# Kernel optimization log

Measured on AMD Instinct MI355X. Metric: run time of the kernel, lower is better.

Reference implementation:

```python
import jax, jax.numpy as jnp
import numpy as np
from jax import lax

Z_DIM = 64
ZS_SIZE = [[1, 1]] * 12 + [[2, 1]] + [[2, 2]] * 11 + [[4, 2]] + [[4, 4]] * 11  # 36 embeddings
FILTER = [[16, 16]] * 6 + [[16, 32]] + [[32, 32]] * 5 + [[32, 64]] + [[64, 64]] * 5  # 18 blocks
OFFS = np.cumsum([0] + [h * k for h, k in ZS_SIZE]).tolist()  # 242 z-vectors total


def _hyper(Z, hn_w2, hn_b2, hn_w1, hn_b1):
    # Batched HyperNetwork: Z [n, 64] -> kernels [n, 16, 16, 3, 3]
    n = Z.shape[0]
    h_in = (Z @ hn_w2 + hn_b2).reshape(n, 16, Z_DIM)            # [n, 16, 64]
    h_fin = jnp.einsum('nid,do->nio', h_in, hn_w1) + hn_b1       # [n, 16, 144]
    return h_fin.reshape(n, 16, 16, 3, 3)


def _make_w(z_all, idx, hn_w2, hn_b2, hn_w1, hn_b1):
    # Assemble conv weight [h*16, k*16, 3, 3] from h*k hypernet tiles (cat dim=1 over k, dim=0 over h)
    h, k = ZS_SIZE[idx]
    Z = z_all[OFFS[idx]:OFFS[idx] + h * k]
    K = _hyper(Z, hn_w2, hn_b2, hn_w1, hn_b1)                    # [h*k, 16, 16, 3, 3]
    K = K.reshape(h, k, 16, 16, 3, 3).transpose(0, 2, 1, 3, 4, 5)
    return K.reshape(h * 16, k * 16, 3, 3)


def _conv(x, w, stride, pad):
    return lax.conv_general_dilated(x, w, (stride, stride), [(pad, pad), (pad, pad)],
                                    dimension_numbers=('NCHW', 'OIHW', 'NCHW'))


def _bn(x, i, g, b, m, v):
    # eval-mode BatchNorm2d with running stats; params padded to 64 channels
    C = x.shape[1]
    gg = g[i, :C].reshape(1, C, 1, 1)
    bb = b[i, :C].reshape(1, C, 1, 1)
    mm = m[i, :C].reshape(1, C, 1, 1)
    vv = v[i, :C].reshape(1, C, 1, 1)
    return (x - mm) * (gg * lax.rsqrt(vv + 1e-5)) + bb


def setup_inputs() -> dict:
    key = jax.random.key(0)
    ks = jax.random.split(key, 16)
    B = 1024
    x = jax.random.normal(ks[0], (B, 3, 32, 32), jnp.float32)
    conv1_w = jax.random.normal(ks[1], (16, 3, 3, 3), jnp.float32) / np.float32(np.sqrt(27.0))
    conv1_b = jnp.zeros((16,), jnp.float32)
    n_bn = 37  # bn1 + 2 per block
    bn_gamma = jnp.ones((n_bn, 64), jnp.float32)
    bn_beta = jnp.zeros((n_bn, 64), jnp.float32)
    bn_mean = jnp.zeros((n_bn, 64), jnp.float32)
    bn_var = jnp.ones((n_bn, 64), jnp.float32)
    hn_w2 = jax.random.normal(ks[2], (Z_DIM, 16 * Z_DIM), jnp.float32) * 0.04
    hn_b2 = jax.random.normal(ks[3], (16 * Z_DIM,), jnp.float32) * 0.01
    hn_w1 = jax.random.normal(ks[4], (Z_DIM, 16 * 9), jnp.float32) * 0.04
    hn_b1 = jax.random.normal(ks[5], (16 * 9,), jnp.float32) * 0.01
    z_all = jax.random.normal(ks[6], (OFFS[-1], Z_DIM), jnp.float32)
    res_w6 = jax.random.normal(ks[7], (32, 16, 1, 1), jnp.float32) * 0.25
    res_b6 = jnp.zeros((32,), jnp.float32)
    res_w12 = jax.random.normal(ks[8], (64, 32, 1, 1), jnp.float32) * 0.18
    res_b12 = jnp.zeros((64,), jnp.float32)
    fin_w = jax.random.normal(ks[9], (10, 64), jnp.float32) * 0.1
    fin_b = jnp.zeros((10,), jnp.float32)
    return {"x": x, "conv1_w": conv1_w, "conv1_b": conv1_b,
            "bn_gamma": bn_gamma, "bn_beta": bn_beta, "bn_mean": bn_mean, "bn_var": bn_var,
            "hn_w2": hn_w2, "hn_b2": hn_b2, "hn_w1": hn_w1, "hn_b1": hn_b1,
            "z_all": z_all, "res_w6": res_w6, "res_b6": res_b6,
            "res_w12": res_w12, "res_b12": res_b12, "fin_w": fin_w, "fin_b": fin_b}


def reference(x, conv1_w, conv1_b, bn_gamma, bn_beta, bn_mean, bn_var,
              hn_w2, hn_b2, hn_w1, hn_b1, z_all,
              res_w6, res_b6, res_w12, res_b12, fin_w, fin_b):
    x = _conv(x, conv1_w, 1, 1) + conv1_b.reshape(1, -1, 1, 1)
    x = jax.nn.relu(_bn(x, 0, bn_gamma, bn_beta, bn_mean, bn_var))
    for i in range(18):
        w1 = _make_w(z_all, 2 * i, hn_w2, hn_b2, hn_w1, hn_b1)
        w2 = _make_w(z_all, 2 * i + 1, hn_w2, hn_b2, hn_w1, hn_b1)
        down = (i > 5 and i % 6 == 0)
        if down:
            rw, rb = (res_w6, res_b6) if i == 6 else (res_w12, res_b12)
            res = _conv(x, rw, 2, 0) + rb.reshape(1, -1, 1, 1)
            stride = 2
        else:
            res = x
            stride = 1
        out = jax.nn.relu(_bn(_conv(x, w1, stride, 1), 1 + 2 * i, bn_gamma, bn_beta, bn_mean, bn_var))
        out = _bn(_conv(out, w2, 1, 1), 2 + 2 * i, bn_gamma, bn_beta, bn_mean, bn_var)
        x = jax.nn.relu(out + res)
    x = x.mean(axis=(2, 3))  # AvgPool2d(8) on [B,64,8,8]
    return x @ fin_w.T + fin_b
```

## Files before the change

kernel.cpp:

```cpp
#include <hip/hip_runtime.h>
#include <hip/hip_bf16.h>


typedef __attribute__((ext_vector_type(8))) short bf16x8;
typedef __attribute__((ext_vector_type(4))) float f32x4;
typedef __attribute__((ext_vector_type(16))) float f32x16;
typedef unsigned short ushort_t;

#define OFFS_LIST {0,1,2,3,4,5,6,7,8,9,10,11,12,14,18,22,26,30,34,38,42,46,50,54,58,66,82,98,114,130,146,162,178,194,210,226,242}
#define K_LIST    {1,1,1,1,1,1,1,1,1,1,1,1,1,2,2,2,2,2,2,2,2,2,2,2,2,4,4,4,4,4,4,4,4,4,4,4}
#define H_LIST    {1,1,1,1,1,1,1,1,1,1,1,1,2,2,2,2,2,2,2,2,2,2,2,2,4,4,4,4,4,4,4,4,4,4,4,4}
#define WOFF_LIST {0,2304,4608,6912,9216,11520,13824,16128,18432,20736,23040,25344,27648,32256,41472,50688,59904,69120,78336,87552,96768,105984,115200,124416,133632,152064,188928,225792,262656,299520,336384,373248,410112,446976,483840,520704}
#define CIN_LIST  {16,16,16,16,16,16,16,16,16,16,16,16,16,32,32,32,32,32,32,32,32,32,32,32,32,64,64,64,64,64,64,64,64,64,64,64}
#define COUT_LIST {16,16,16,16,16,16,16,16,16,16,16,16,32,32,32,32,32,32,32,32,32,32,32,32,64,64,64,64,64,64,64,64,64,64,64,64}
#define WFOFF_LIST {0,7680,15360,23040,30720,38400,46080,53760,61440,69120,76800,84480,92160,107520,135168,165888,196608,227328,258048,288768,319488,350208,380928,411648,442368,503808,632832,755712,878592,1001472,1124352,1247232,1370112,1492992,1615872,1738752}

__constant__ int d_offs[37]  = OFFS_LIST;
__constant__ int d_k[36]     = K_LIST;
__constant__ int d_hh[36]    = H_LIST;
__constant__ int d_woff[36]  = WOFF_LIST;
__constant__ int d_cin[36]   = CIN_LIST;
__constant__ int d_cout[36]  = COUT_LIST;
__constant__ int d_wfoff[36] = WFOFF_LIST;

__device__ inline void split3(float x, ushort_t& h, ushort_t& m, ushort_t& l) {
    unsigned xb = __float_as_uint(x);
    unsigned hb = (xb + 0x8000u) >> 16;
    float fh = __uint_as_float(hb << 16);
    float r = x - fh;
    unsigned mb = (__float_as_uint(r) + 0x8000u) >> 16;
    float fm = __uint_as_float(mb << 16);
    float r2 = r - fm;
    unsigned lb = (__float_as_uint(r2) + 0x8000u) >> 16;
    h = (ushort_t)hb; m = (ushort_t)mb; l = (ushort_t)lb;
}

__global__ void prep(const float* __restrict__ g, const float* __restrict__ be,
                     const float* __restrict__ m, const float* __restrict__ v,
                     const float* __restrict__ rw6, const float* __restrict__ rb12,
                     float* __restrict__ sc, float* __restrict__ sh,
                     float* __restrict__ rwT6, float* __restrict__ shp25) {
    int i = blockIdx.x * blockDim.x + threadIdx.x;
    if (i < 2368) {
        float s = g[i] * rsqrtf(v[i] + 1e-5f);
        sc[i] = s;
        sh[i] = be[i] - m[i] * s;
    } else if (i < 2368 + 512) {
        int t = i - 2368;
        int co = t % 32, ci = t / 32;
        rwT6[ci * 32 + co] = rw6[co * 16 + ci];
    } else if (i < 2368 + 512 + 64) {
        int c = i - 2880;
        int idx2 = 26 * 64 + c;
        float s = g[idx2] * rsqrtf(v[idx2] + 1e-5f);
        shp25[c] = be[idx2] - m[idx2] * s + rb12[c];
    }
}

__global__ void hyper_kernel(const float* __restrict__ z_all, const float* __restrict__ w2,
                             const float* __restrict__ b2, const float* __restrict__ w1,
                             const float* __restrict__ b1, const float* __restrict__ bnsc,
                             float* __restrict__ Wg) {
    int n = blockIdx.x;
    int tid = threadIdx.x;
    __shared__ float zrow[64];
    __shared__ float hin[1024];
    if (tid < 64) zrow[tid] = z_all[n * 64 + tid];
    __syncthreads();
    for (int mcol = tid; mcol < 1024; mcol += 256) {
        float acc = b2[mcol];
        #pragma unroll 8
        for (int d = 0; d < 64; ++d) acc += zrow[d] * w2[d * 1024 + mcol];
        hin[mcol] = acc;
    }
    __syncthreads();
    int L = 0;
    while (n >= d_offs[L + 1]) ++L;
    int r = n - d_offs[L];
    int kk = d_k[L];
    int a = r / kk, bb = r % kk;
    int Cin = kk * 16;
    int Cout = d_hh[L] * 16;
    const float* scp = bnsc + (L + 1) * 64;
    float* wp = Wg + d_woff[L];
    for (int e = tid; e < 2304; e += 256) {
        int i = e / 144, o = e % 144;
        int j = o / 9, tap = o % 9;
        float acc = b1[o];
        #pragma unroll 8
        for (int d = 0; d < 64; ++d) acc += hin[i * 64 + d] * w1[d * 144 + o];
        int co = a * 16 + i;
        acc *= scp[co];
        wp[(tap * Cin + (bb * 16 + j)) * Cout + co] = acc;
    }
}

__global__ void split_w(const float* __restrict__ Wg, const float* __restrict__ rw12,
                        ushort_t* __restrict__ Wf) {
    int L = blockIdx.y;
    int CIN = d_cin[L], COUT = d_cout[L];
    int idx = blockIdx.x * 256 + threadIdx.x;
    int j = idx & 7, lane = (idx >> 3) & 63, t = idx >> 9;
    int hi = lane >> 5;
    float wv;
    int base;
    if (L < 14) {
        int K = 9 * CIN, NKS = (K + 31) / 32, NT = COUT / 16;
        if (t >= NKS * NT) return;
        int nt = t % NT, ks = t / NT;
        int k = ks * 32 + (lane >> 4) * 8 + j;
        int co = nt * 16 + (lane & 15);
        wv = (k < K) ? Wg[d_woff[L] + k * COUT + co] : 0.f;
        base = d_wfoff[L] + ((ks * NT + nt) * 3) * 512 + lane * 8 + j;
    } else {
        int CG8 = CIN / 8, NKS = 5 * CG8, NT = COUT / 32;
        int TKS = NKS + ((L == 25) ? 2 : 0);
        if (t >= TKS * NT) return;
        int nt = t % NT, ks = t / NT;
        int co = nt * 32 + (lane & 31);
        if (ks < NKS) {
            int o = 2 * ks + hi, tap = o % 10, c8 = o / 10;
            int ci = c8 * 8 + j;
            wv = (tap < 9) ? Wg[d_woff[L] + (tap * CIN + ci) * COUT + co] : 0.f;
        } else {
            int k = (ks - NKS) * 16 + hi * 8 + j;
            wv = rw12[co * 32 + k];
        }
        base = d_wfoff[L] + ((ks * NT + nt) * 3) * 512 + lane * 8 + j;
    }
    ushort_t h, m, l;
    split3(wv, h, m, l);
    Wf[base] = h; Wf[base + 512] = m; Wf[base + 1024] = l;
}

__global__ void conv_first(const float* __restrict__ x, const float* __restrict__ cw,
                           const float* __restrict__ cb, const float* __restrict__ g,
                           const float* __restrict__ be, const float* __restrict__ m,
                           const float* __restrict__ v, float* __restrict__ out) {
    int idx = blockIdx.x * 256 + threadIdx.x;
    int px = idx & 31; int t = idx >> 5;
    int py = t & 31;   int b = t >> 5;
    float acc[16];
    #pragma unroll
    for (int co = 0; co < 16; ++co) acc[co] = 0.f;
    const float* ip = x + (long)b * 3 * 1024;
    #pragma unroll 1
    for (int ci = 0; ci < 3; ++ci) {
        #pragma unroll 1
        for (int ky = 0; ky < 3; ++ky) {
            int iy = py + ky - 1;
            if ((unsigned)iy >= 32u) continue;
            #pragma unroll
            for (int kx = 0; kx < 3; ++kx) {
                int ix = px + kx - 1;
                if ((unsigned)ix < 32u) {
                    float xv = ip[ci * 1024 + iy * 32 + ix];
                    #pragma unroll
                    for (int co = 0; co < 16; ++co)
                        acc[co] += xv * cw[co * 27 + ci * 9 + ky * 3 + kx];
                }
            }
        }
    }
    long o = ((long)(b * 32 + py) * 32 + px) * 16;
    #pragma unroll
    for (int co = 0; co < 16; ++co) {
        float s = g[co] * rsqrtf(v[co] + 1e-5f);
        float val = (acc[co] + cb[co] - m[co]) * s + be[co];
        out[o + co] = fmaxf(val, 0.f);
    }
}

__global__ void pad_zero_f32(float* __restrict__ buf, int H2, int C4) {
    int idx = blockIdx.x * 256 + threadIdx.x;
    int nb = 2 * H2 + 2 * (H2 - 2);
    int total = 1024 * nb * C4;
    if (idx >= total) return;
    int ch = idx % C4; int t = idx / C4;
    int bp = t % nb; int img = t / nb;
    int y, x;
    if (bp < H2) { y = 0; x = bp; }
    else if (bp < 2 * H2) { y = H2 - 1; x = bp - H2; }
    else { int s = bp - 2 * H2; y = 1 + (s >> 1); x = (s & 1) ? H2 - 1 : 0; }
    long off = (((long)img * H2 + y) * H2 + x) * (C4 * 4) + ch * 4;
    *(float4*)(buf + off) = make_float4(0.f, 0.f, 0.f, 0.f);
}

template<int CIN, int COUT, int HIN, int STRIDE, int TH, int TW, int MODE, int CR, int HR, int OUTF>
__global__ __launch_bounds__(256) void conv_mfma(
        const float* __restrict__ in, const ushort_t* __restrict__ wf,
        const float* __restrict__ shp, const float* __restrict__ res,
        const float* __restrict__ rwT, const float* __restrict__ rb,
        float* __restrict__ out) {
    constexpr int HOUT = HIN / STRIDE;
    constexpr int H2O = HOUT + 2;
    constexpr int CG8 = CIN / 8;
    constexpr int IH = (TH - 1) * STRIDE + 3;
    constexpr int IW = (TW - 1) * STRIDE + 3;
    constexpr int K = 9 * CIN;
    constexpr int NKS = (K + 31) / 32;
    constexpr bool TAIL = (K % 32) != 0;
    constexpr int NT = COUT / 16;
    constexpr int NMT = TH * TW / 16;
    constexpr int MTW = NMT / 4;
    constexpr int PADC = ((2 - (IH * IW)) % 8 + 8) % 8;
    constexpr int CSTU = IH * IW + PADC;
    constexpr int PST = CG8 * CSTU;
    constexpr int TX = HOUT / TW, TY = HOUT / TH;

    __shared__ uint4 lds[3 * PST];

    int tid = threadIdx.x;
    int bid = blockIdx.x;
    int tile = bid % (TY * TX);
    int b = bid / (TY * TX);
    int ty = tile / TX, tx = tile % TX;
    int Y0 = ty * TH, X0 = tx * TW;
    int gy0 = Y0 * STRIDE - 1, gx0 = X0 * STRIDE - 1;

    for (int e = tid; e < CG8 * IH * IW; e += 256) {
        int c8 = e / (IH * IW); int rr = e % (IH * IW);
        int ly = rr / IW, lx = rr % IW;
        int gy = gy0 + ly, gx = gx0 + lx;
        float vv[8];
        if ((unsigned)gy < (unsigned)HIN && (unsigned)gx < (unsigned)HIN) {
            const float4* p = (const float4*)(in + ((long)(b * HIN + gy) * HIN + gx) * CIN + c8 * 8);
            float4 a0 = p[0], a1 = p[1];
            vv[0]=a0.x; vv[1]=a0.y; vv[2]=a0.z; vv[3]=a0.w;
            vv[4]=a1.x; vv[5]=a1.y; vv[6]=a1.z; vv[7]=a1.w;
        } else {
            #pragma unroll
            for (int q = 0; q < 8; ++q) vv[q] = 0.f;
        }
        union { ushort_t u[8]; uint4 q4; } H, M, L;
        #pragma unroll
        for (int q = 0; q < 8; ++q) split3(vv[q], H.u[q], M.u[q], L.u[q]);
        int a16 = c8 * CSTU + rr;
        lds[a16] = H.q4; lds[PST + a16] = M.q4; lds[2 * PST + a16] = L.q4;
    }
    __syncthreads();

    int lane = tid & 63, wid = tid >> 6;
    int g = lane >> 4, r16 = lane & 15;

    f32x4 acc[MTW][NT] = {};

    int pbase[MTW];
    #pragma unroll
    for (int mt = 0; mt < MTW; ++mt) {
        int pid = (wid + 4 * mt) * 16 + r16;
        int py = pid / TW, px = pid % TW;
        pbase[mt] = (py * STRIDE) * IW + px * STRIDE;
    }

    #pragma unroll
    for (int ks = 0; ks < NKS; ++ks) {
        bf16x8 bfr[NT][3];
        #pragma unroll
        for (int nt = 0; nt < NT; ++nt)
            #pragma unroll
            for (int p = 0; p < 3; ++p)
                bfr[nt][p] = *(const bf16x8*)(wf + ((ks * NT + nt) * 3 + p) * 512 + lane * 8);

        int k0 = ks * 32 + g * 8;
        int tap = k0 / CIN;
        int ci8 = (k0 % CIN) >> 3;
        int ky = (tap * 11) >> 5;
        int kx = tap - 3 * ky;
        int ofs = ci8 * CSTU + ky * IW + kx;

        #pragma unroll
        for (int mt = 0; mt < MTW; ++mt) {
            int e16 = ofs + pbase[mt];
            if (TAIL && ks == NKS - 1) e16 = (g < 2) ? e16 : 0;
            const uint4* ap = lds + e16;
            bf16x8 ah = *(const bf16x8*)(ap);
            bf16x8 am = *(const bf16x8*)(ap + PST);
            bf16x8 al = *(const bf16x8*)(ap + 2 * PST);
            #pragma unroll
            for (int nt = 0; nt < NT; ++nt) {
                f32x4 c = acc[mt][nt];
                c = __builtin_amdgcn_mfma_f32_16x16x32_bf16(ah, bfr[nt][0], c, 0, 0, 0);
                c = __builtin_amdgcn_mfma_f32_16x16x32_bf16(ah, bfr[nt][1], c, 0, 0, 0);
                c = __builtin_amdgcn_mfma_f32_16x16x32_bf16(am, bfr[nt][0], c, 0, 0, 0);
                c = __builtin_amdgcn_mfma_f32_16x16x32_bf16(ah, bfr[nt][2], c, 0, 0, 0);
                c = __builtin_amdgcn_mfma_f32_16x16x32_bf16(am, bfr[nt][1], c, 0, 0, 0);
                c = __builtin_amdgcn_mfma_f32_16x16x32_bf16(al, bfr[nt][0], c, 0, 0, 0);
                acc[mt][nt] = c;
            }
        }
    }

    #pragma unroll
    for (int mt = 0; mt < MTW; ++mt) {
        #pragma unroll
        for (int nt = 0; nt < NT; ++nt) {
            int co = nt * 16 + r16;
            float shv = shp[co];
            #pragma unroll
            for (int reg = 0; reg < 4; ++reg) {
                int pid = (wid + 4 * mt) * 16 + g * 4 + reg;
                int py = pid / TW, px = pid % TW;
                int gy = Y0 + py, gx = X0 + px;
                float val = acc[mt][nt][reg] + shv;
                if (MODE == 1) {
                    long oidx = ((long)(b * HOUT + gy) * HOUT + gx) * COUT + co;
                    val += res[oidx];
                }
                if (MODE == 2) {
                    float racc = rb[co];
                    const float* rp = res + ((long)(b * HR + 2 * gy) * HR + 2 * gx) * CR;
                    #pragma unroll 4
                    for (int ci = 0; ci < CR; ++ci) racc += rp[ci] * rwT[ci * COUT + co];
                    val += racc;
                }
                val = fmaxf(val, 0.f);
                if (OUTF == 0) {
                    long oidx = ((long)(b * HOUT + gy) * HOUT + gx) * COUT + co;
                    out[oidx] = val;
                } else {
                    out[(((long)b * H2O + gy + 1) * H2O + gx + 1) * COUT + co] = val;
                }
            }
        }
    }
}

template<int CIN, int COUT, int HIN, int STRIDE, int PXB, int MODE, int RKS, int CHUNK>
__global__ __launch_bounds__(256) void conv_s23(
        const float* __restrict__ in, const ushort_t* __restrict__ wf,
        const float* __restrict__ shp, const float* __restrict__ res,
        float* __restrict__ out) {
    constexpr int HOUT = HIN / STRIDE;
    constexpr int H2I = HIN + 2, H2O = HOUT + 2;
    constexpr int C8 = CIN / 8;
    constexpr int NKS = 5 * C8;
    constexpr int TKS = NKS + RKS;
    constexpr int NC = TKS / CHUNK;
    constexpr int NTT = COUT / 32;
    constexpr int ROWSB = PXB / HOUT;
    constexpr int SLABR = (ROWSB - 1) * STRIDE + 3;
    constexpr int SLABPIX = SLABR * H2I;
    constexpr int NBLK = HOUT / ROWSB;
    constexpr int RESU = 3 * C8 * SLABPIX;
    constexpr int LDSU = RESU + ((MODE == 2) ? 12 * 64 : 0);

    __shared__ uint4 lds[LDSU];

    int tid = threadIdx.x, lane = tid & 63, wid = tid >> 6;
    int lp = lane & 31, hi = lane >> 5;
    int bid = blockIdx.x;
    int img = bid / NBLK, blocky = bid % NBLK;
    int pxg = wid / NTT, ntb = wid % NTT;
    int pix0 = pxg * 32 + lp;
    int py_blk = pix0 / HOUT, px = pix0 % HOUT;
    int py = blocky * ROWSB + py_blk;
    int slabrow0 = blocky * ROWSB * STRIDE;

    const ushort_t* wfl = wf + lane * 8;

    bf16x8 wA[CHUNK][3], wB[CHUNK][3];
    auto LW = [&](int c, bf16x8 (&w)[CHUNK][3]) {
        #pragma unroll
        for (int i = 0; i < CHUNK; ++i) {
            int ks = c * CHUNK + i;
            #pragma unroll
            for (int pp = 0; pp < 3; ++pp)
                w[i][pp] = *(const bf16x8*)(wfl + ((ks * NTT + ntb) * 3 + pp) * 512);
        }
    };

    LW(0, wA);
    if (NC > 1) LW(1, wB);

    const float* ib = in + (long)img * H2I * H2I * CIN;
    for (int it = tid; it < SLABPIX * C8; it += 256) {
        int pix = it % SLABPIX, cc = it / SLABPIX;
        int sr = pix / H2I, sc = pix % H2I;
        const float* p4 = ib + ((long)(slabrow0 + sr) * H2I + sc) * CIN + cc * 8;
        float4 a0 = ((const float4*)p4)[0], a1 = ((const float4*)p4)[1];
        float vv[8] = {a0.x, a0.y, a0.z, a0.w, a1.x, a1.y, a1.z, a1.w};
        union { ushort_t u[8]; uint4 q; } H, M, L;
        #pragma unroll
        for (int q = 0; q < 8; ++q) split3(vv[q], H.u[q], M.u[q], L.u[q]);
        int u0 = cc * 3;
        lds[u0 * SLABPIX + pix] = H.q;
        lds[(u0 + 1) * SLABPIX + pix] = M.q;
        lds[(u0 + 2) * SLABPIX + pix] = L.q;
    }
    if (MODE == 2) {
        for (int it = tid; it < 256; it += 256) {
            int pix = it & 63, cc = it >> 6;
            int ry = pix >> 3, rx = pix & 7;
            const float* r4 = res + (((long)img * 18 + (2 * ry + 1)) * 18 + (2 * rx + 1)) * 32 + cc * 8;
            float4 a0 = ((const float4*)r4)[0], a1 = ((const float4*)r4)[1];
            float vv[8] = {a0.x, a0.y, a0.z, a0.w, a1.x, a1.y, a1.z, a1.w};
            union { ushort_t u[8]; uint4 q; } H, M, L;
            #pragma unroll
            for (int q = 0; q < 8; ++q) split3(vv[q], H.u[q], M.u[q], L.u[q]);
            int u0 = RESU + cc * 3 * 64;
            lds[u0 + pix] = H.q;
            lds[u0 + 64 + pix] = M.q;
            lds[u0 + 128 + pix] = L.q;
        }
    }
    __syncthreads();

    int pbase = (py_blk * STRIDE) * H2I + px * STRIDE;
    f32x16 acc = {};

    auto DOC = [&](int c, bf16x8 (&w)[CHUNK][3]) {
        #pragma unroll
        for (int i = 0; i < CHUNK; ++i) {
            int ks = c * CHUNK + i;
            bf16x8 x0, x1, x2;
            if (RKS > 0 && ks >= NKS) {
                int o2 = 2 * (ks - NKS) + hi;
                int a = RESU + o2 * 3 * 64 + pix0;
                x0 = *(const bf16x8*)&lds[a];
                x1 = *(const bf16x8*)&lds[a + 64];
                x2 = *(const bf16x8*)&lds[a + 128];
            } else {
                int o = 2 * ks + hi;
                int tap = o % 10, c8i = o / 10;
                int ky = (tap * 11) >> 5, kx = tap - 3 * ky;
                int t16 = (tap == 9) ? 0 : (ky * H2I + kx);
                int a = (c8i * 3) * SLABPIX + pbase + t16;
                x0 = *(const bf16x8*)&lds[a];
                x1 = *(const bf16x8*)&lds[a + SLABPIX];
                x2 = *(const bf16x8*)&lds[a + 2 * SLABPIX];
            }
            acc = __builtin_amdgcn_mfma_f32_32x32x16_bf16(w[i][0], x0, acc, 0, 0, 0);
            acc = __builtin_amdgcn_mfma_f32_32x32x16_bf16(w[i][1], x0, acc, 0, 0, 0);
            acc = __builtin_amdgcn_mfma_f32_32x32x16_bf16(w[i][0], x1, acc, 0, 0, 0);
            acc = __builtin_amdgcn_mfma_f32_32x32x16_bf16(w[i][2], x0, acc, 0, 0, 0);
            acc = __builtin_amdgcn_mfma_f32_32x32x16_bf16(w[i][1], x1, acc, 0, 0, 0);
            acc = __builtin_amdgcn_mfma_f32_32x32x16_bf16(w[i][0], x2, acc, 0, 0, 0);
        }
    };

    #pragma unroll 1
    for (int c = 0; c < NC; c += 2) {
        DOC(c, wA);
        if (c + 2 < NC) LW(c + 2, wA);
        if (c + 1 < NC) DOC(c + 1, wB);
        if (c + 3 < NC) LW(c + 3, wB);
    }

    float* ob = out + (((long)img * H2O + py + 1) * H2O + (px + 1)) * COUT;
    const float* rb4 = (MODE == 1)
        ? res + (((long)img * H2O + py + 1) * H2O + (px + 1)) * COUT : nullptr;
    #pragma unroll
    for (int g = 0; g < 4; ++g) {
        int co = ntb * 32 + g * 8 + 4 * hi;
        float v0 = acc[4 * g + 0] + shp[co + 0];
        float v1 = acc[4 * g + 1] + shp[co + 1];
        float v2 = acc[4 * g + 2] + shp[co + 2];
        float v3 = acc[4 * g + 3] + shp[co + 3];
        if (MODE == 1) {
            float4 r = *(const float4*)(rb4 + co);
            v0 += r.x; v1 += r.y; v2 += r.z; v3 += r.w;
        }
        *(float4*)(ob + co) = make_float4(fmaxf(v0, 0.f), fmaxf(v1, 0.f),
                                          fmaxf(v2, 0.f), fmaxf(v3, 0.f));
    }
}

__global__ void pool_fc(const float* __restrict__ X, const float* __restrict__ fw,
                        const float* __restrict__ fb, float* __restrict__ out) {
    int b = blockIdx.x;
    int c = threadIdx.x;
    float s = 0.f;
    #pragma unroll
    for (int p = 0; p < 64; ++p) {
        int y = p >> 3, x = p & 7;
        s += X[(((long)b * 10 + y + 1) * 10 + (x + 1)) * 64 + c];
    }
    __shared__ float pooled[64];
    pooled[c] = s * (1.f / 64.f);
    __syncthreads();
    if (c < 10) {
        float acc = fb[c];
        #pragma unroll
        for (int k = 0; k < 64; ++k) acc += pooled[k] * fw[c * 64 + k];
        out[b * 10 + c] = acc;
    }
}

extern "C" void kernel_launch(void* const* d_in, const int* in_sizes, int n_in,
                              void* d_out, int out_size, void* d_ws, size_t ws_size,
                              hipStream_t stream) {
    const float* x       = (const float*)d_in[0];
    const float* conv1_w = (const float*)d_in[1];
    const float* conv1_b = (const float*)d_in[2];
    const float* bn_g    = (const float*)d_in[3];
    const float* bn_b    = (const float*)d_in[4];
    const float* bn_m    = (const float*)d_in[5];
    const float* bn_v    = (const float*)d_in[6];
    const float* hn_w2   = (const float*)d_in[7];
    const float* hn_b2   = (const float*)d_in[8];
    const float* hn_w1   = (const float*)d_in[9];
    const float* hn_b1   = (const float*)d_in[10];
    const float* z_all   = (const float*)d_in[11];
    const float* res_w6  = (const float*)d_in[12];
    const float* res_b6  = (const float*)d_in[13];
    const float* res_w12 = (const float*)d_in[14];
    const float* res_b12 = (const float*)d_in[15];
    const float* fin_w   = (const float*)d_in[16];
    const float* fin_b   = (const float*)d_in[17];
    float* outp = (float*)d_out;

    float* wsf      = (float*)d_ws;
    float* Wg       = wsf;
    float* bnsc     = wsf + 557568;
    float* bnsh     = wsf + 559936;
    float* rwT6     = wsf + 562304;
    float* shp25    = wsf + 564864;
    ushort_t* Wfrag = (ushort_t*)(wsf + 565248);

    float* A0f = (float*)((char*)d_ws + (size_t)(16) * (1 << 20));
    float* A1f = (float*)((char*)d_ws + (size_t)(80) * (1 << 20));
    float* A2f = (float*)((char*)d_ws + (size_t)(144) * (1 << 20));

    static const int wfoff[36] = WFOFF_LIST;

    prep<<<20, 256, 0, stream>>>(bn_g, bn_b, bn_m, bn_v, res_w6, res_b12,
                                 bnsc, bnsh, rwT6, shp25);
    hyper_kernel<<<242, 256, 0, stream>>>(z_all, hn_w2, hn_b2, hn_w1, hn_b1, bnsc, Wg);
    split_w<<<dim3(168, 36), 256, 0, stream>>>(Wg, res_w12, Wfrag);
    conv_first<<<4096, 256, 0, stream>>>(x, conv1_w, conv1_b, bn_g, bn_b, bn_m, bn_v, A0f);

    float* X = A0f; float* T1 = A1f; float* T2 = A2f;
    for (int i = 0; i < 6; ++i) {
        int L1 = 2 * i, L2 = 2 * i + 1;
        conv_mfma<16,16,32,1,16,16,0,1,1,0><<<4096, 256, 0, stream>>>(
            X, Wfrag + wfoff[L1], bnsh + (L1 + 1) * 64, nullptr, nullptr, nullptr, T1);
        conv_mfma<16,16,32,1,16,16,1,1,1,0><<<4096, 256, 0, stream>>>(
            T1, Wfrag + wfoff[L2], bnsh + (L2 + 1) * 64, X, nullptr, nullptr, T2);
        float* tmp = X; X = T2; T2 = tmp;
    }
    conv_mfma<16,32,32,2,8,16,0,1,1,0><<<2048, 256, 0, stream>>>(
        A0f, Wfrag + wfoff[12], bnsh + 13 * 64, nullptr, nullptr, nullptr, A1f);
    pad_zero_f32<<<2176, 256, 0, stream>>>(A2f, 18, 8);
    conv_mfma<32,32,16,1,8,16,2,16,32,2><<<2048, 256, 0, stream>>>(
        A1f, Wfrag + wfoff[13], bnsh + 14 * 64, A0f, rwT6, res_b6, A2f);
    pad_zero_f32<<<2176, 256, 0, stream>>>(A1f, 18, 8);
    pad_zero_f32<<<2176, 256, 0, stream>>>(A0f, 18, 8);

    X = A2f; T1 = A1f; T2 = A0f;
    for (int i = 7; i < 12; ++i) {
        int L1 = 2 * i, L2 = 2 * i + 1;
        conv_s23<32,32,16,1,128,0,0,5><<<2048, 256, 0, stream>>>(
            X, Wfrag + wfoff[L1], bnsh + (L1 + 1) * 64, nullptr, T1);
        conv_s23<32,32,16,1,128,1,0,5><<<2048, 256, 0, stream>>>(
            T1, Wfrag + wfoff[L2], bnsh + (L2 + 1) * 64, X, T2);
        float* tmp = X; X = T2; T2 = tmp;
    }
    pad_zero_f32<<<2304, 256, 0, stream>>>(A1f, 10, 16);
    conv_s23<32,64,16,2,64,0,0,5><<<1024, 256, 0, stream>>>(
        A0f, Wfrag + wfoff[24], bnsh + 25 * 64, nullptr, A1f);
    pad_zero_f32<<<2304, 256, 0, stream>>>(A2f, 10, 16);
    conv_s23<64,64,8,1,64,2,2,6><<<1024, 256, 0, stream>>>(
        A1f, Wfrag + wfoff[25], shp25, A0f, A2f);
    pad_zero_f32<<<2304, 256, 0, stream>>>(A0f, 10, 16);

    X = A2f; T1 = A1f; T2 = A0f;
    for (int i = 13; i < 18; ++i) {
        int L1 = 2 * i, L2 = 2 * i + 1;
        conv_s23<64,64,8,1,64,0,0,5><<<1024, 256, 0, stream>>>(
            X, Wfrag + wfoff[L1], bnsh + (L1 + 1) * 64, nullptr, T1);
        conv_s23<64,64,8,1,64,1,0,5><<<1024, 256, 0, stream>>>(
            T1, Wfrag + wfoff[L2], bnsh + (L2 + 1) * 64, X, T2);
        float* tmp = X; X = T2; T2 = tmp;
    }
    pool_fc<<<1024, 64, 0, stream>>>(A0f, fin_w, fin_b, outp);
}
```

Measured before the change: 1.468 ms.

## Add specialized stage-1 16-channel conv kernel with row-slab LDS tiling

Introduces conv_s1, a kernel dedicated to the 16->16 channel, 32x32 stride-1 convolutions. Each block processes an 8-row slab of one image and stages a 10x34 padded window in LDS, already split into three bf16 parts. Weight fragments are preloaded into registers, and six MFMAs per k-step give a three-way split-bf16 approximation of fp32. The aim is to cut the generic conv_mfma template's overhead and improve LDS reuse for these 12 launches. In exchange, the halo rows are reloaded for every slab, and the fragment/tap index mapping is hand-coded and must match the weight layout.

```diff
diff --git a/kernel.cpp b/kernel.cpp
--- a/kernel.cpp
+++ b/kernel.cpp
@@ -186,6 +186,108 @@
     *(float4*)(buf + off) = make_float4(0.f, 0.f, 0.f, 0.f);
 }
 
+template<int MODE>
+__global__ __launch_bounds__(256) void conv_s1(
+        const float* __restrict__ in, const ushort_t* __restrict__ wf,
+        const float* __restrict__ shp, const float* __restrict__ res,
+        float* __restrict__ out) {
+    constexpr int W2 = 34, SLABPIX = 10 * W2;
+    constexpr int NKS = 5;
+
+    __shared__ uint4 lds[6 * SLABPIX];
+
+    int tid = threadIdx.x, lane = tid & 63, wid = tid >> 6;
+    int g = lane >> 4, r16 = lane & 15;
+    int bid = blockIdx.x;
+    int img = bid >> 2, blocky = bid & 3;
+    int row0 = blocky * 8;
+
+    const ushort_t* wfl = wf + lane * 8;
+    bf16x8 wv[NKS][3];
+    #pragma unroll
+    for (int ks = 0; ks < NKS; ++ks)
+        #pragma unroll
+        for (int p = 0; p < 3; ++p)
+            wv[ks][p] = *(const bf16x8*)(wfl + (ks * 3 + p) * 512);
+    #pragma unroll
+    for (int ks = 0; ks < NKS; ++ks)
+        #pragma unroll
+        for (int p = 0; p < 3; ++p)
+            asm volatile("" : "+v"(wv[ks][p]));
+
+    const float* ib = in + (long)img * (32 * 32 * 16);
+    for (int it = tid; it < SLABPIX * 2; it += 256) {
+        int pix = it % SLABPIX, cc = it / SLABPIX;
+        int sr = pix / W2, sc = pix % W2;
+        int gy = row0 - 1 + sr, gx = sc - 1;
+        float vv[8];
+        if ((unsigned)gy < 32u && (unsigned)gx < 32u) {
+            const float4* p4 = (const float4*)(ib + ((long)gy * 32 + gx) * 16 + cc * 8);
+            float4 a0 = p4[0], a1 = p4[1];
+            vv[0]=a0.x; vv[1]=a0.y; vv[2]=a0.z; vv[3]=a0.w;
+            vv[4]=a1.x; vv[5]=a1.y; vv[6]=a1.z; vv[7]=a1.w;
+        } else {
+            #pragma unroll
+            for (int q = 0; q < 8; ++q) vv[q] = 0.f;
+        }
+        union { ushort_t u[8]; uint4 q; } H, M, L;
+        #pragma unroll
+        for (int q = 0; q < 8; ++q) split3(vv[q], H.u[q], M.u[q], L.u[q]);
+        lds[(cc * 3 + 0) * SLABPIX + pix] = H.q;
+        lds[(cc * 3 + 1) * SLABPIX + pix] = M.q;
+        lds[(cc * 3 + 2) * SLABPIX + pix] = L.q;
+    }
+    __syncthreads();
+
+    int pbase[4];
+    #pragma unroll
+    for (int mt = 0; mt < 4; ++mt) {
+        int pid = (wid * 4 + mt) * 16 + r16;
+        pbase[mt] = (pid >> 5) * W2 + (pid & 31);
+    }
+
+    f32x4 acc[4] = {};
+
+    #pragma unroll
+    for (int ks = 0; ks < NKS; ++ks) {
+        int k0 = ks * 32 + g * 8;
+        int tap = k0 >> 4;
+        int ci8 = (k0 >> 3) & 1;
+        int ky = (tap * 11) >> 5;
+        int kx = tap - 3 * ky;
+        bool dead = (ks == NKS - 1) && (g >= 2);
+        int ofs = dead ? 0 : (ci8 * 3) * SLABPIX + ky * W2 + kx;
+        #pragma unroll
+        for (int mt = 0; mt < 4; ++mt) {
+            int e16 = dead ? 0 : ofs + pbase[mt];
+            bf16x8 ah = *(const bf16x8*)&lds[e16];
+            bf16x8 am = *(const bf16x8*)&lds[e16 + SLABPIX];
+            bf16x8 al = *(const bf16x8*)&lds[e16 + 2 * SLABPIX];
+            f32x4 c = acc[mt];
+            c = __builtin_amdgcn_mfma_f32_16x16x32_bf16(ah, wv[ks][0], c, 0, 0, 0);
+            c = __builtin_amdgcn_mfma_f32_16x16x32_bf16(ah, wv[ks][1], c, 0, 0, 0);
+            c = __builtin_amdgcn_mfma_f32_16x16x32_bf16(am, wv[ks][0], c, 0, 0, 0);
+            c = __builtin_amdgcn_mfma_f32_16x16x32_bf16(ah, wv[ks][2], c, 0, 0, 0);
+            c = __builtin_amdgcn_mfma_f32_16x16x32_bf16(am, wv[ks][1], c, 0, 0, 0);
+            c = __builtin_amdgcn_mfma_f32_16x16x32_bf16(al, wv[ks][0], c, 0, 0, 0);
+            acc[mt] = c;
+        }
+    }
+
+    #pragma unroll
+    for (int mt = 0; mt < 4; ++mt) {
+        #pragma unroll
+        for (int reg = 0; reg < 4; ++reg) {
+            int pid = (wid * 4 + mt) * 16 + g * 4 + reg;
+            int gy = row0 + (pid >> 5), gx = pid & 31;
+            long oidx = (((long)img * 32 + gy) * 32 + gx) * 16 + r16;
+            float val = acc[mt][reg] + shp[r16];
+            if (MODE == 1) val += res[oidx];
+            out[oidx] = fmaxf(val, 0.f);
+        }
+    }
+}
+
 template<int CIN, int COUT, int HIN, int STRIDE, int TH, int TW, int MODE, int CR, int HR, int OUTF>
 __global__ __launch_bounds__(256) void conv_mfma(
         const float* __restrict__ in, const ushort_t* __restrict__ wf,
@@ -533,10 +635,10 @@
     float* X = A0f; float* T1 = A1f; float* T2 = A2f;
     for (int i = 0; i < 6; ++i) {
         int L1 = 2 * i, L2 = 2 * i + 1;
-        conv_mfma<16,16,32,1,16,16,0,1,1,0><<<4096, 256, 0, stream>>>(
-            X, Wfrag + wfoff[L1], bnsh + (L1 + 1) * 64, nullptr, nullptr, nullptr, T1);
-        conv_mfma<16,16,32,1,16,16,1,1,1,0><<<4096, 256, 0, stream>>>(
-            T1, Wfrag + wfoff[L2], bnsh + (L2 + 1) * 64, X, nullptr, nullptr, T2);
+        conv_s1<0><<<4096, 256, 0, stream>>>(
+            X, Wfrag + wfoff[L1], bnsh + (L1 + 1) * 64, nullptr, T1);
+        conv_s1<1><<<4096, 256, 0, stream>>>(
+            T1, Wfrag + wfoff[L2], bnsh + (L2 + 1) * 64, X, T2);
         float* tmp = X; X = T2; T2 = tmp;
     }
     conv_mfma<16,32,32,2,8,16,0,1,1,0><<<2048, 256, 0, stream>>>(
```

Measured after the change: 1.477 ms. About the same (+0.6%).
